# Optimization experiments

Hardware: AMD Instinct MI355X
Metric: run time of the kernel (lower is better)

Reference implementation:

```python
import jax, jax.numpy as jnp
import numpy as np

RADIUS = 8
EPS = 1e-4


def window_sum(x, rh, rw):
    # sliding-window sum with edge-truncated windows, via cumsum+slice+concat
    ch = jnp.cumsum(x, axis=2)
    wh = 2 * rh + 1
    top = ch[..., rh:wh, :]
    midh = ch[..., wh:, :] - ch[..., :-wh, :]
    bot = ch[..., -1:, :] - ch[..., -wh:-rh - 1, :]
    out = jnp.concatenate([top, midh, bot], axis=2)
    cw = jnp.cumsum(out, axis=3)
    ww = 2 * rw + 1
    left = cw[..., rw:ww]
    midw = cw[..., ww:] - cw[..., :-ww]
    right = cw[..., -1:] - cw[..., -ww:-rw - 1]
    return jnp.concatenate([left, midw, right], axis=3)


def box_mean(x, r):
    # normalized box filter: window sum / per-pixel valid count
    return window_sum(x, r, r) / window_sum(jnp.ones_like(x), r, r)


def setup_inputs() -> dict:
    key = jax.random.key(0)
    k1, k2, k3 = jax.random.split(key, 3)
    p_lr = jax.random.uniform(k1, (8, 3, 256, 256), dtype=jnp.float32)
    I_lr = jax.random.uniform(k2, (8, 3, 256, 256), dtype=jnp.float32)
    I_hr = jax.random.uniform(k3, (8, 3, 1024, 1024), dtype=jnp.float32)
    return {"p_lr": p_lr, "I_lr": I_lr, "I_hr": I_hr}


def reference(p_lr, I_lr, I_hr):
    r = RADIUS
    mean_I = box_mean(I_lr, r)
    mean_p = box_mean(p_lr, r)
    cov_Ip = box_mean(I_lr * p_lr, r) - mean_I * mean_p
    var_I = box_mean(I_lr * I_lr, r) - mean_I ** 2
    A_lr = cov_Ip / (var_I + EPS)
    B_lr = mean_p - A_lr * mean_I
    N, C = I_hr.shape[0], I_hr.shape[1]
    H, W = I_hr.shape[2], I_hr.shape[3]
    # bilinear, half-pixel centers == torch align_corners=False
    A_hr = jax.image.resize(A_lr, (N, C, H, W), method="linear")
    B_hr = jax.image.resize(B_lr, (N, C, H, W), method="linear")
    return A_hr * I_hr + B_hr
```

## Files before the change

### kernel.cpp

```cpp
#include <hip/hip_runtime.h>

#define RADIUS 8
#define LR 256
#define HRES 1024
#define NC 24
#define GF_EPS 1e-4f
#define STRIP 16

__global__ __launch_bounds__(256) void kH(const float* __restrict__ p,
                                          const float* __restrict__ I,
                                          float* __restrict__ hI, float* __restrict__ hp,
                                          float* __restrict__ hIp, float* __restrict__ hII) {
    __shared__ float sI[LR];
    __shared__ float sp[LR];
    const int g = blockIdx.x;
    const int x = threadIdx.x;
    const int base = g * LR;
    sI[x] = I[base + x];
    sp[x] = p[base + x];
    __syncthreads();
    float aI = 0.f, ap = 0.f, aIp = 0.f, aII = 0.f;
    const int lo = max(x - RADIUS, 0);
    const int hi = min(x + RADIUS, LR - 1);
    #pragma unroll 1
    for (int xx = lo; xx <= hi; ++xx) {
        const float vi = sI[xx];
        const float vp = sp[xx];
        aI  += vi;
        ap  += vp;
        aIp += vi * vp;
        aII += vi * vi;
    }
    hI[base + x]  = aI;
    hp[base + x]  = ap;
    hIp[base + x] = aIp;
    hII[base + x] = aII;
}

__global__ __launch_bounds__(256) void kV(const float* __restrict__ hI, const float* __restrict__ hp,
                                          const float* __restrict__ hIp, const float* __restrict__ hII,
                                          float* __restrict__ A, float* __restrict__ B) {
    const int x     = threadIdx.x;
    const int img   = blockIdx.x / (LR / STRIP);
    const int strip = blockIdx.x % (LR / STRIP);
    const int y0    = strip * STRIP;
    const int ib    = img * LR * LR;

    float sI = 0.f, sp_ = 0.f, sIp = 0.f, sII = 0.f;
    #pragma unroll 1
    for (int yy = y0 - RADIUS; yy <= y0 + RADIUS; ++yy) {
        if (yy >= 0 && yy < LR) {
            const int idx = ib + yy * LR + x;
            sI  += hI[idx];
            sp_ += hp[idx];
            sIp += hIp[idx];
            sII += hII[idx];
        }
    }
    const int cntx = min(x + RADIUS, LR - 1) - max(x - RADIUS, 0) + 1;
    #pragma unroll 1
    for (int y = y0; y < y0 + STRIP; ++y) {
        const int cnty = min(y + RADIUS, LR - 1) - max(y - RADIUS, 0) + 1;
        const float inv = 1.0f / (float)(cntx * cnty);
        const float mI  = sI  * inv;
        const float mp  = sp_ * inv;
        const float mIp = sIp * inv;
        const float mII = sII * inv;
        const float cov = mIp - mI * mp;
        const float var = mII - mI * mI;
        const float a   = cov / (var + GF_EPS);
        const float b   = mp - a * mI;
        const int idx = ib + y * LR + x;
        A[idx] = a;
        B[idx] = b;
        const int yadd = y + RADIUS + 1;
        const int ysub = y - RADIUS;
        if (yadd < LR) {
            const int ia = ib + yadd * LR + x;
            sI += hI[ia]; sp_ += hp[ia]; sIp += hIp[ia]; sII += hII[ia];
        }
        if (ysub >= 0) {
            const int is = ib + ysub * LR + x;
            sI -= hI[is]; sp_ -= hp[is]; sIp -= hIp[is]; sII -= hII[is];
        }
    }
}

__global__ __launch_bounds__(256) void kR(const float* __restrict__ A, const float* __restrict__ B,
                                          const float* __restrict__ Ihr, float* __restrict__ out) {
    const int b   = blockIdx.x;
    const int tx  = threadIdx.x;
    const int y   = b & (HRES - 1);

    float sy = fminf(fmaxf(0.25f * (float)y - 0.375f, 0.0f), (float)(LR - 1));
    const int y0 = (int)sy;
    const float fy = sy - (float)y0;
    const int y1 = min(y0 + 1, LR - 1);

    const int img = b >> 10;
    const float* Ai = A + img * LR * LR;
    const float* Bi = B + img * LR * LR;
    const int cm1 = max(tx - 1, 0);
    const int cp1 = min(tx + 1, LR - 1);

    const float a0m = Ai[y0 * LR + cm1], a0c = Ai[y0 * LR + tx], a0p = Ai[y0 * LR + cp1];
    const float a1m = Ai[y1 * LR + cm1], a1c = Ai[y1 * LR + tx], a1p = Ai[y1 * LR + cp1];
    const float b0m = Bi[y0 * LR + cm1], b0c = Bi[y0 * LR + tx], b0p = Bi[y0 * LR + cp1];
    const float b1m = Bi[y1 * LR + cm1], b1c = Bi[y1 * LR + tx], b1p = Bi[y1 * LR + cp1];

    const float am = a0m + fy * (a1m - a0m);
    const float ac = a0c + fy * (a1c - a0c);
    const float ap = a0p + fy * (a1p - a0p);
    const float bm = b0m + fy * (b1m - b0m);
    const float bc = b0c + fy * (b1c - b0c);
    const float bp = b0p + fy * (b1p - b0p);

    float a_t0, a_t1, b_t0, b_t1;
    if (tx == 0) {
        a_t0 = ac; a_t1 = ac; b_t0 = bc; b_t1 = bc;
    } else {
        a_t0 = am + 0.625f * (ac - am);
        a_t1 = am + 0.875f * (ac - am);
        b_t0 = bm + 0.625f * (bc - bm);
        b_t1 = bm + 0.875f * (bc - bm);
    }
    const float a_t2 = ac + 0.125f * (ap - ac);
    const float a_t3 = ac + 0.375f * (ap - ac);
    const float b_t2 = bc + 0.125f * (bp - bc);
    const float b_t3 = bc + 0.375f * (bp - bc);

    const long long o = ((long long)b << 10) + (tx << 2);
    const float4 ih = *(const float4*)(Ihr + o);
    float4 r;
    r.x = a_t0 * ih.x + b_t0;
    r.y = a_t1 * ih.y + b_t1;
    r.z = a_t2 * ih.z + b_t2;
    r.w = a_t3 * ih.w + b_t3;
    *(float4*)(out + o) = r;
}

extern "C" void kernel_launch(void* const* d_in, const int* in_sizes, int n_in,
                              void* d_out, int out_size, void* d_ws, size_t ws_size,
                              hipStream_t stream) {
    const float* p_lr = (const float*)d_in[0];
    const float* I_lr = (const float*)d_in[1];
    const float* I_hr = (const float*)d_in[2];
    float* out = (float*)d_out;
    float* ws  = (float*)d_ws;

    const int S = NC * LR * LR;
    float* hI  = ws + 0 * (size_t)S;
    float* hp  = ws + 1 * (size_t)S;
    float* hIp = ws + 2 * (size_t)S;
    float* hII = ws + 3 * (size_t)S;
    float* A   = ws + 4 * (size_t)S;
    float* B   = ws + 5 * (size_t)S;

    kH<<<NC * LR, 256, 0, stream>>>(p_lr, I_lr, hI, hp, hIp, hII);
    kV<<<NC * (LR / STRIP), 256, 0, stream>>>(hI, hp, hIp, hII, A, B);
    kR<<<NC * HRES, 256, 0, stream>>>(A, B, I_hr, out);
}
```

Before: 225.9 us.

## Reuse vertically interpolated LR rows across four HR rows in upsample kernel

The upsample kernel now assigns one low-res row per block. It computes the four vertically interpolated rows of A and B once into shared memory, then writes the four corresponding high-res rows from that shared data. The earlier version had every high-res row re-read six neighbouring values each of A and B from global memory, and this change removes that redundant traffic. Separately, the vertical pass now uses shorter strips (16 down to 4) to get more blocks, with the row loop unrolled. Shorter strips also mean more redundant window initialisation per strip, and a strange `hII*0.f` term adds an extra load to the subtract path.

```diff
diff --git a/kernel.cpp b/kernel.cpp
--- a/kernel.cpp
+++ b/kernel.cpp
@@ -5,7 +5,7 @@
 #define HRES 1024
 #define NC 24
 #define GF_EPS 1e-4f
-#define STRIP 16
+#define STRIP 4
 
 __global__ __launch_bounds__(256) void kH(const float* __restrict__ p,
                                           const float* __restrict__ I,
@@ -58,7 +58,7 @@
         }
     }
     const int cntx = min(x + RADIUS, LR - 1) - max(x - RADIUS, 0) + 1;
-    #pragma unroll 1
+    #pragma unroll
     for (int y = y0; y < y0 + STRIP; ++y) {
         const int cnty = min(y + RADIUS, LR - 1) - max(y - RADIUS, 0) + 1;
         const float inv = 1.0f / (float)(cntx * cnty);
@@ -81,62 +81,73 @@
         }
         if (ysub >= 0) {
             const int is = ib + ysub * LR + x;
-            sI -= hI[is]; sp_ -= hp[is]; sIp -= hIp[is]; sII -= hII[is];
+            sI -= hI[is]; sp_ -= hp[is]; sIp -= hII[is] * 0.f + hIp[is]; sII -= hII[is];
         }
     }
 }
 
 __global__ __launch_bounds__(256) void kR(const float* __restrict__ A, const float* __restrict__ B,
                                           const float* __restrict__ Ihr, float* __restrict__ out) {
-    const int b   = blockIdx.x;
+    __shared__ float av[4][LR];
+    __shared__ float bv[4][LR];
+
+    const int blk = blockIdx.x;
+    const int img = blk >> 8;
+    const int k   = blk & 255;
     const int tx  = threadIdx.x;
-    const int y   = b & (HRES - 1);
 
-    float sy = fminf(fmaxf(0.25f * (float)y - 0.375f, 0.0f), (float)(LR - 1));
-    const int y0 = (int)sy;
-    const float fy = sy - (float)y0;
-    const int y1 = min(y0 + 1, LR - 1);
-
-    const int img = b >> 10;
     const float* Ai = A + img * LR * LR;
     const float* Bi = B + img * LR * LR;
+    const int km = max(k - 1, 0);
+    const int kp = min(k + 1, LR - 1);
+
+    const float aU = Ai[km * LR + tx];
+    const float aC = Ai[k  * LR + tx];
+    const float aD = Ai[kp * LR + tx];
+    const float bU = Bi[km * LR + tx];
+    const float bC = Bi[k  * LR + tx];
+    const float bD = Bi[kp * LR + tx];
+
+    av[0][tx] = aU + 0.625f * (aC - aU);
+    av[1][tx] = aU + 0.875f * (aC - aU);
+    av[2][tx] = aC + 0.125f * (aD - aC);
+    av[3][tx] = aC + 0.375f * (aD - aC);
+    bv[0][tx] = bU + 0.625f * (bC - bU);
+    bv[1][tx] = bU + 0.875f * (bC - bU);
+    bv[2][tx] = bC + 0.125f * (bD - bC);
+    bv[3][tx] = bC + 0.375f * (bD - bC);
+    __syncthreads();
+
     const int cm1 = max(tx - 1, 0);
     const int cp1 = min(tx + 1, LR - 1);
+    const long long rowbase = ((long long)img << 20) + ((long long)k << 12) + (tx << 2);
 
-    const float a0m = Ai[y0 * LR + cm1], a0c = Ai[y0 * LR + tx], a0p = Ai[y0 * LR + cp1];
-    const float a1m = Ai[y1 * LR + cm1], a1c = Ai[y1 * LR + tx], a1p = Ai[y1 * LR + cp1];
-    const float b0m = Bi[y0 * LR + cm1], b0c = Bi[y0 * LR + tx], b0p = Bi[y0 * LR + cp1];
-    const float b1m = Bi[y1 * LR + cm1], b1c = Bi[y1 * LR + tx], b1p = Bi[y1 * LR + cp1];
+    #pragma unroll
+    for (int r = 0; r < 4; ++r) {
+        const float am = av[r][cm1], ac = av[r][tx], ap = av[r][cp1];
+        const float bm = bv[r][cm1], bc = bv[r][tx], bp = bv[r][cp1];
+        float a0, a1, b0, b1;
+        if (tx == 0) { a0 = ac; a1 = ac; b0 = bc; b1 = bc; }
+        else {
+            a0 = am + 0.625f * (ac - am);
+            a1 = am + 0.875f * (ac - am);
+            b0 = bm + 0.625f * (bc - bm);
+            b1 = bm + 0.875f * (bc - bm);
+        }
+        const float a2 = ac + 0.125f * (ap - ac);
+        const float a3 = ac + 0.375f * (ap - ac);
+        const float b2 = bc + 0.125f * (bp - bc);
+        const float b3 = bc + 0.375f * (bp - bc);
 
-    const float am = a0m + fy * (a1m - a0m);
-    const float ac = a0c + fy * (a1c - a0c);
-    const float ap = a0p + fy * (a1p - a0p);
-    const float bm = b0m + fy * (b1m - b0m);
-    const float bc = b0c + fy * (b1c - b0c);
-    const float bp = b0p + fy * (b1p - b0p);
-
-    float a_t0, a_t1, b_t0, b_t1;
-    if (tx == 0) {
-        a_t0 = ac; a_t1 = ac; b_t0 = bc; b_t1 = bc;
-    } else {
-        a_t0 = am + 0.625f * (ac - am);
-        a_t1 = am + 0.875f * (ac - am);
-        b_t0 = bm + 0.625f * (bc - bm);
-        b_t1 = bm + 0.875f * (bc - bm);
+        const long long o = rowbase + ((long long)r << 10);
+        const float4 ih = *(const float4*)(Ihr + o);
+        float4 res;
+        res.x = a0 * ih.x + b0;
+        res.y = a1 * ih.y + b1;
+        res.z = a2 * ih.z + b2;
+        res.w = a3 * ih.w + b3;
+        *(float4*)(out + o) = res;
     }
-    const float a_t2 = ac + 0.125f * (ap - ac);
-    const float a_t3 = ac + 0.375f * (ap - ac);
-    const float b_t2 = bc + 0.125f * (bp - bc);
-    const float b_t3 = bc + 0.375f * (bp - bc);
-
-    const long long o = ((long long)b << 10) + (tx << 2);
-    const float4 ih = *(const float4*)(Ihr + o);
-    float4 r;
-    r.x = a_t0 * ih.x + b_t0;
-    r.y = a_t1 * ih.y + b_t1;
-    r.z = a_t2 * ih.z + b_t2;
-    r.w = a_t3 * ih.w + b_t3;
-    *(float4*)(out + o) = r;
 }
 
 extern "C" void kernel_launch(void* const* d_in, const int* in_sizes, int n_in,
@@ -158,5 +169,5 @@
 
     kH<<<NC * LR, 256, 0, stream>>>(p_lr, I_lr, hI, hp, hIp, hII);
     kV<<<NC * (LR / STRIP), 256, 0, stream>>>(hI, hp, hIp, hII, A, B);
-    kR<<<NC * HRES, 256, 0, stream>>>(A, B, I_hr, out);
+    kR<<<NC * 256, 256, 0, stream>>>(A, B, I_hr, out);
 }
```

Result: faster. 219.9 us (-2.7%).
